# Performance work log

Measured on AMD Instinct MI355X. Metric: run time of the kernel, lower is better.

The kernel has to match this reference:

```python
import jax, jax.numpy as jnp
import numpy as np

H = 512      # hidden_size
GH = 512     # global_hidden_size
V = 128      # VOCAB_SIZE (one-hot arg_hot width)
D = 14       # tree depth; complete binary tree
NUM_OPS = 36
N_INT = 5    # num_internal_ops
N_NODES = 2 ** (D + 1) - 1  # 32767, heap layout: node i has children 2i+1, 2i+2


def _p(key, i, shape, s=0.05):
    return jax.random.normal(jax.random.fold_in(key, i), shape, dtype=jnp.float32) * s


def setup_inputs() -> dict:
    key = jax.random.key(0)
    return {
        "tokens": jax.random.randint(jax.random.fold_in(key, 0), (N_NODES,), 0, V),
        "validity_mask": jnp.ones((NUM_OPS,), jnp.float32),
        # binary tree-LSTM (blstm): 2 children
        "W_iou_b": _p(key, 1, (V, 3 * H)), "U_iou_b": _p(key, 2, (2, H, 3 * H)), "b_iou_b": jnp.zeros((3 * H,), jnp.float32),
        "Wf_b": _p(key, 3, (V, H)), "Uf_b": _p(key, 4, (2, H, H)), "bf_b": jnp.ones((H,), jnp.float32),
        # ternary tree-LSTM (tlstm): 3 children
        "W_iou_t": _p(key, 5, (V, 3 * H)), "U_iou_t": _p(key, 6, (3, H, 3 * H)), "b_iou_t": jnp.zeros((3 * H,), jnp.float32),
        "Wf_t": _p(key, 7, (V, H)), "Uf_t": _p(key, 8, (3, H, H)), "bf_t": jnp.ones((H,), jnp.float32),
        # FFN: one h-by-h layer (ffn_complexity = h^2 * n_layers, n_layers=1)
        "ffn_W": _p(key, 9, (H, H)), "ffn_b": jnp.zeros((H,), jnp.float32),
        # global LSTM (1 layer, 1 step), torch gate order i,f,g,o
        "lstm_Wx": _p(key, 10, (H, 4 * GH)), "lstm_Wh": _p(key, 11, (GH, 4 * GH)), "lstm_b": jnp.zeros((4 * GH,), jnp.float32),
        # actor heads on concat(root_hidden, h_glob)
        "hl_W": _p(key, 12, (H + GH, 2)), "hl_b": jnp.zeros((2,), jnp.float32),
        "int_W": _p(key, 13, (H + GH, N_INT)), "int_b": jnp.zeros((N_INT,), jnp.float32),
        "act_W": _p(key, 14, (H + GH, NUM_OPS)), "act_b": jnp.zeros((NUM_OPS,), jnp.float32),
    }


def _nary_cell(x, hk, ck, W_iou, U_iou, b_iou, Wf, Uf, bf):
    # x: [n, V]; hk, ck: [n, K, H]  (K children)
    iou = x @ W_iou + jnp.einsum('nkh,khg->ng', hk, U_iou) + b_iou
    i, o, u = jnp.split(iou, 3, axis=-1)
    f = jax.nn.sigmoid((x @ Wf + bf)[:, None, :] + jnp.einsum('nkh,khg->nkg', hk, Uf))
    c = jax.nn.sigmoid(i) * jnp.tanh(u) + jnp.sum(f * ck, axis=1)
    h = jax.nn.sigmoid(o) * jnp.tanh(c)
    return h, c


def _forward(tokens, validity_mask, W_iou_b, U_iou_b, b_iou_b, Wf_b, Uf_b, bf_b,
             W_iou_t, U_iou_t, b_iou_t, Wf_t, Uf_t, bf_t, ffn_W, ffn_b,
             lstm_Wx, lstm_Wh, lstm_b, hl_W, hl_b, int_W, int_b, act_W, act_b):
    arg_hot = jax.nn.one_hot(tokens, V, dtype=jnp.float32)  # [N_NODES, V]
    h_prev = c_prev = None
    h_ab = c_ab = None
    # apply_binary_lstm over the whole tree, bottom-up, one batched cell per level
    for lvl in range(D, -1, -1):
        n = 2 ** lvl
        x = arg_hot[n - 1:2 * n - 1]  # level lvl occupies heap slots [2^l-1, 2^{l+1}-2]
        if h_prev is None:
            hk = jnp.zeros((n, 2, H), jnp.float32)  # leaves: tz children
            ck = hk
        else:
            hk = h_prev.reshape(n, 2, H)
            ck = c_prev.reshape(n, 2, H)
        h_prev, c_prev = _nary_cell(x, hk, ck, W_iou_b, U_iou_b, b_iou_b, Wf_b, Uf_b, bf_b)
        if lvl == 1:
            h_ab, c_ab = h_prev, c_prev  # root's children a, b
    # apply_ternary_lstm at depth 0: children = (self.hidden, a.hidden, b.hidden)
    hk3 = jnp.concatenate([h_prev, h_ab], axis=0)[None]  # [1, 3, H]
    ck3 = jnp.concatenate([c_prev, c_ab], axis=0)[None]
    h_root, c_root = _nary_cell(arg_hot[0:1], hk3, ck3, W_iou_t, U_iou_t, b_iou_t, Wf_t, Uf_t, bf_t)
    # apply_ffn (1 layer) then apply_global_lstm (single step from zero state)
    h_f = jnp.maximum(h_root @ ffn_W + ffn_b, 0.0)  # [1, H]
    h_g = jnp.zeros((1, GH), jnp.float32)
    c_g = h_g
    gates = h_f @ lstm_Wx + h_g @ lstm_Wh + lstm_b
    gi, gf, gg, go = jnp.split(gates, 4, axis=-1)
    c_g = jax.nn.sigmoid(gf) * c_g + jax.nn.sigmoid(gi) * jnp.tanh(gg)
    h_g = jax.nn.sigmoid(go) * jnp.tanh(c_g)
    # actor heads
    feat = jnp.concatenate([h_f, h_g], axis=-1)  # [1, H+GH]
    hl = feat @ hl_W + hl_b
    il = feat @ int_W + int_b
    el = jnp.log(validity_mask)[None, :] + feat @ (act_W * validity_mask[None, :]) + act_b * validity_mask
    return jnp.concatenate([hl, il, el], axis=-1)  # [1, 2 + N_INT + NUM_OPS]


def reference(tokens, validity_mask, W_iou_b, U_iou_b, b_iou_b, Wf_b, Uf_b, bf_b,
              W_iou_t, U_iou_t, b_iou_t, Wf_t, Uf_t, bf_t, ffn_W, ffn_b,
              lstm_Wx, lstm_Wh, lstm_b, hl_W, hl_b, int_W, int_b, act_W, act_b):
    return _forward(tokens, validity_mask, W_iou_b, U_iou_b, b_iou_b, Wf_b, Uf_b, bf_b,
                    W_iou_t, U_iou_t, b_iou_t, Wf_t, Uf_t, bf_t, ffn_W, ffn_b,
                    lstm_Wx, lstm_Wh, lstm_b, hl_W, hl_b, int_W, int_b, act_W, act_b)
```

## Files before the change

kernel.cpp:

```cpp
#include <hip/hip_runtime.h>
#include <hip/hip_bf16.h>
#include <math.h>

#define H 512
#define V 128
#define NLEAF 16384

typedef __attribute__((ext_vector_type(4))) float f32x4;
typedef __attribute__((ext_vector_type(8))) short s16x8;
typedef __attribute__((ext_vector_type(4))) unsigned short u16x4;
typedef unsigned short ushort_t;

__device__ ushort_t g_hb0[NLEAF * H];
__device__ ushort_t g_hb1[(NLEAF / 2) * H];
__device__ float    g_c0[NLEAF * H];
__device__ float    g_c1[(NLEAF / 2) * H];
__device__ __align__(16) ushort_t g_htab[V * H];
__device__ __align__(16) float    g_ctab[V * H];
__device__ __align__(16) float    g_Wpack[V * H * 4];
__device__ __align__(16) float    g_Uh0[V * 3 * H];
__device__ __align__(16) float    g_Uh1[V * 3 * H];
__device__ __align__(16) float    g_Vf0[V * H];
__device__ __align__(16) float    g_Vf1[V * H];
__device__ __align__(16) float    g_uhp[4 * 2 * V * 2048];
__device__ ushort_t g_UiouT[3 * H * 2 * H];
__device__ ushort_t g_UfT[H * 2 * H];
__device__ __align__(16) ushort_t g_Ustage[8 * 16 * 32 * 64 * 8];
__device__ ushort_t g_UiouTt[3 * H * 3 * H];
__device__ ushort_t g_UfTt[H * 3 * H];
__device__ float    g_rpart[3 * 3072];
__device__ float    g_hf[H];
__device__ float    g_gates[4 * H];

__device__ __forceinline__ float sigm(float x) { return 1.0f / (1.0f + __expf(-x)); }
__device__ __forceinline__ float ftanh(float x) {
  return 1.0f - 2.0f / (__expf(2.0f * x) + 1.0f);
}
__device__ __forceinline__ ushort_t f2bf(float x) {
  __hip_bfloat16 b = __float2bfloat16(x);
  return *reinterpret_cast<ushort_t*>(&b);
}
__device__ __forceinline__ float bf2f(ushort_t u) {
  union { unsigned int i; float f; } v; v.i = ((unsigned int)u) << 16; return v.f;
}
__device__ __forceinline__ void gload_lds16(const void* g, void* l) {
  __builtin_amdgcn_global_load_lds(
      (const __attribute__((address_space(1))) unsigned int*)g,
      (__attribute__((address_space(3))) unsigned int*)l, 16, 0, 0);
}
#define WAITV(N) asm volatile("s_waitcnt vmcnt(" #N ")" ::: "memory")

__global__ __launch_bounds__(256) void k_prep(
    const float* __restrict__ s0, const float* __restrict__ s1,
    const float* __restrict__ s2, const float* __restrict__ s3,
    ushort_t* __restrict__ d0, ushort_t* __restrict__ d1,
    ushort_t* __restrict__ d2, ushort_t* __restrict__ d3,
    const float* __restrict__ Wiou, const float* __restrict__ biou,
    const float* __restrict__ Wf, const float* __restrict__ bf) {
  if (blockIdx.z == 4) {
    const int v = blockIdx.y * 48 + blockIdx.x;
    if (v >= V) return;
    for (int j = threadIdx.x; j < H; j += 256) {
      float wi = Wiou[(size_t)v * 1536 + j] + biou[j];
      float wo = Wiou[(size_t)v * 1536 + 512 + j] + biou[512 + j];
      float wu = Wiou[(size_t)v * 1536 + 1024 + j] + biou[1024 + j];
      float wf = Wf[(size_t)v * 512 + j] + bf[j];
      f32x4 wp = {wi, wo, wu, wf};
      *reinterpret_cast<f32x4*>(&g_Wpack[((size_t)v * 512 + j) * 4]) = wp;
      float c = sigm(wi) * ftanh(wu);
      float h = sigm(wo) * ftanh(c);
      g_htab[v * H + j] = f2bf(h);
      g_ctab[v * H + j] = c;
    }
    return;
  }
  const float* src; ushort_t* dst; int R, Cc;
  switch (blockIdx.z) {
    case 0: src = s0; dst = d0; R = 1024; Cc = 1536; break;
    case 1: src = s1; dst = d1; R = 1024; Cc = 512; break;
    case 2: src = s2; dst = d2; R = 1536; Cc = 1536; break;
    default: src = s3; dst = d3; R = 1536; Cc = 512; break;
  }
  int bc = blockIdx.x * 32, br = blockIdx.y * 32;
  if (bc >= Cc || br >= R) return;
  __shared__ float t[32][33];
  int tx = threadIdx.x & 31, ty = threadIdx.x >> 5;
  for (int rr = ty; rr < 32; rr += 8)
    t[rr][tx] = src[(size_t)(br + rr) * Cc + bc + tx];
  __syncthreads();
  for (int rr = ty; rr < 32; rr += 8)
    dst[(size_t)(bc + rr) * R + br + tx] = f2bf(t[tx][rr]);
}

__global__ __launch_bounds__(256) void k_packU(const float* __restrict__ Uiou,
                                               const float* __restrict__ Uf) {
  const int jb = blockIdx.x;
  const int ct = blockIdx.y;
  const int kz = blockIdx.z;
  const int t = threadIdx.x;
  const int kt = kz * 4 + (t >> 6);
  const int lane = t & 63;
  const int colu = ct * 16 + (lane & 15);
  const int g = colu >> 6;
  const int jj = jb * 64 + (colu & 63);
  const int kbase = kt * 32 + ((lane >> 4) << 3);
  u16x4 v0, v1;
  #pragma unroll
  for (int r = 0; r < 8; ++r) {
    int k = kbase + r;
    float v = (g < 3) ? Uiou[(size_t)k * 1536 + g * 512 + jj]
                      : Uf[(size_t)k * 512 + jj];
    if (r < 4) v0[r] = f2bf(v); else v1[r - 4] = f2bf(v);
  }
  ushort_t* dst = g_Ustage + (((size_t)(jb * 16 + ct) * 32 + kt) * 64 + lane) * 8;
  *reinterpret_cast<u16x4*>(dst) = v0;
  *reinterpret_cast<u16x4*>(dst + 4) = v1;
}

__global__ __launch_bounds__(256) void k_uhg() {
  const int cb0 = blockIdx.x * 64;
  const int kh = blockIdx.y;
  const int kc = blockIdx.z;
  const int tid = threadIdx.x;
  const int lane = tid & 63;
  const int w = tid >> 6;
  const int wry = w >> 1;
  const int cx = w & 1;

  __shared__ f32x4 suv[3072];
  char* smem = (char*)suv;

  const unsigned kA = (unsigned)(kc * 256) + ((lane >> 4) * 16);
  const unsigned kB = (unsigned)(kh * 1024) + kA;
  #pragma unroll
  for (int uu = 0; uu < 3; ++uu) {
    int u = w * 3 + uu;
    const char* base;
    unsigned dstb;
    if (u < 8) {
      int row = u * 16 + (lane & 15);
      base = (const char*)g_htab + (size_t)row * 1024 + kA;
      dstb = (unsigned)u * 4096u;
    } else {
      int col = cb0 + (u - 8) * 16 + (lane & 15);
      const ushort_t* cp = (col < 1536) ? (g_UiouT + (size_t)col * 1024)
                                        : (g_UfT + (size_t)(col - 1536) * 1024);
      base = (const char*)cp + kB;
      dstb = 32768u + (unsigned)(u - 8) * 4096u;
    }
    #pragma unroll
    for (int kt = 0; kt < 4; ++kt)
      gload_lds16(base + kt * 64, smem + dstb + kt * 1024u);
  }
  WAITV(0);
  __syncthreads();

  f32x4 acc[4][2];
  #pragma unroll
  for (int a = 0; a < 4; ++a) { acc[a][0] = (f32x4){0,0,0,0}; acc[a][1] = (f32x4){0,0,0,0}; }

  #pragma unroll
  for (int kt = 0; kt < 4; ++kt) {
    const char* ab = smem + wry * 16384 + kt * 1024 + lane * 16;
    const char* bb = smem + 32768 + cx * 8192 + kt * 1024 + lane * 16;
    s16x8 b0 = *(const s16x8*)(bb);
    s16x8 b1 = *(const s16x8*)(bb + 4096);
    #pragma unroll
    for (int rtl = 0; rtl < 4; ++rtl) {
      s16x8 av = *(const s16x8*)(ab + rtl * 4096);
      acc[rtl][0] = __builtin_amdgcn_mfma_f32_16x16x32_bf16(av, b0, acc[rtl][0], 0, 0, 0);
      acc[rtl][1] = __builtin_amdgcn_mfma_f32_16x16x32_bf16(av, b1, acc[rtl][1], 0, 0, 0);
    }
  }

  float* outb = g_uhp + ((size_t)(kc * 2 + kh) * V) * 2048;
  #pragma unroll
  for (int rtl = 0; rtl < 4; ++rtl) {
    #pragma unroll
    for (int t = 0; t < 2; ++t) {
      int col = cb0 + cx * 32 + t * 16 + (lane & 15);
      int vb = wry * 64 + rtl * 16 + (lane >> 4) * 4;
      #pragma unroll
      for (int r = 0; r < 4; ++r)
        outb[(size_t)(vb + r) * 2048 + col] = acc[rtl][t][r];
    }
  }
}

__global__ __launch_bounds__(256) void k_uhred() {
  int e = blockIdx.x * 256 + threadIdx.x;
  float s = g_uhp[e] + g_uhp[524288 + e] + g_uhp[2 * 524288 + e]
          + g_uhp[3 * 524288 + e];
  int kh = e >> 18;
  int rem = e & 262143;
  int v = rem >> 11;
  int c = rem & 2047;
  if (c < 1536) (kh ? g_Uh1 : g_Uh0)[(size_t)v * 1536 + c] = s;
  else          (kh ? g_Vf1 : g_Vf0)[(size_t)v * 512 + (c - 1536)] = s;
}

__global__ __launch_bounds__(256) void k_top_cell(const int* __restrict__ tokens) {
  const int total = 8192 * 128;
  for (int q = blockIdx.x * 256 + threadIdx.x; q < total; q += gridDim.x * 256) {
    int i = q >> 7, jv = q & 127;
    int t0 = tokens[(NLEAF - 1) + 2 * i];
    int t1 = tokens[(NLEAF - 1) + 2 * i + 1];
    int tk = tokens[8191 + i];
    const f32x4* u0 = (const f32x4*)&g_Uh0[(size_t)t0 * 1536];
    const f32x4* u1 = (const f32x4*)&g_Uh1[(size_t)t1 * 1536];
    f32x4 ii = u0[jv] + u1[jv];
    f32x4 oo = u0[128 + jv] + u1[128 + jv];
    f32x4 uu = u0[256 + jv] + u1[256 + jv];
    f32x4 v0 = ((const f32x4*)&g_Vf0[(size_t)t0 * 512])[jv];
    f32x4 v1 = ((const f32x4*)&g_Vf1[(size_t)t1 * 512])[jv];
    f32x4 c0 = ((const f32x4*)&g_ctab[(size_t)t0 * 512])[jv];
    f32x4 c1 = ((const f32x4*)&g_ctab[(size_t)t1 * 512])[jv];
    const f32x4* wpp = (const f32x4*)g_Wpack + (size_t)tk * 512 + jv * 4;
    u16x4 hv; f32x4 cv;
    #pragma unroll
    for (int r = 0; r < 4; ++r) {
      f32x4 wp = wpp[r];
      float ig = ii[r] + wp[0];
      float og = oo[r] + wp[1];
      float ug = uu[r] + wp[2];
      float fp = wp[3];
      float cc = sigm(ig) * ftanh(ug) + sigm(fp + v0[r]) * c0[r]
               + sigm(fp + v1[r]) * c1[r];
      float hh = sigm(og) * ftanh(cc);
      cv[r] = cc;
      hv[r] = f2bf(hh);
    }
    *reinterpret_cast<u16x4*>(&g_hb1[(size_t)q * 4]) = hv;
    *reinterpret_cast<f32x4*>(&g_c1[(size_t)q * 4]) = cv;
  }
}

#define COMPUTE64(FA, S)                                                     \
  {                                                                          \
    const char* ab = smem + buf * 16384 + wry * 8192 + (S) * 1024 + lane * 16; \
    s16x8 a0 = *(const s16x8*)(ab);                                          \
    s16x8 a1 = *(const s16x8*)(ab + 2048);                                   \
    s16x8 a2 = *(const s16x8*)(ab + 4096);                                   \
    s16x8 a3 = *(const s16x8*)(ab + 6144);                                   \
    const char* bb = smem + 32768 + buf * 32768 + cx * 4096 + (S) * 1024 + lane * 16; \
    s16x8 b0 = *(const s16x8*)(bb);                                          \
    s16x8 b1 = *(const s16x8*)(bb + 2048);                                   \
    s16x8 b2 = *(const s16x8*)(bb + 8192);                                   \
    s16x8 b3 = *(const s16x8*)(bb + 10240);                                  \
    s16x8 b4 = *(const s16x8*)(bb + 16384);                                  \
    s16x8 b5 = *(const s16x8*)(bb + 18432);                                  \
    s16x8 b6 = *(const s16x8*)(bb + 24576);                                  \
    s16x8 b7 = *(const s16x8*)(bb + 26624);                                  \
    s16x8 aa[4] = {a0, a1, a2, a3};                                          \
    _Pragma("unroll")                                                        \
    for (int rtl = 0; rtl < 4; ++rtl) {                                      \
      acc[rtl][0] = __builtin_amdgcn_mfma_f32_16x16x32_bf16(aa[rtl], b0, acc[rtl][0], 0, 0, 0); \
      acc[rtl][1] = __builtin_amdgcn_mfma_f32_16x16x32_bf16(aa[rtl], b1, acc[rtl][1], 0, 0, 0); \
      acc[rtl][2] = __builtin_amdgcn_mfma_f32_16x16x32_bf16(aa[rtl], b2, acc[rtl][2], 0, 0, 0); \
      acc[rtl][3] = __builtin_amdgcn_mfma_f32_16x16x32_bf16(aa[rtl], b3, acc[rtl][3], 0, 0, 0); \
      acc[rtl][4] = __builtin_amdgcn_mfma_f32_16x16x32_bf16(aa[rtl], b4, acc[rtl][4], 0, 0, 0); \
      acc[rtl][5] = __builtin_amdgcn_mfma_f32_16x16x32_bf16(aa[rtl], b5, acc[rtl][5], 0, 0, 0); \
      acc[rtl][FA] = __builtin_amdgcn_mfma_f32_16x16x32_bf16(aa[rtl], b6, acc[rtl][FA], 0, 0, 0); \
      acc[rtl][FA + 1] = __builtin_amdgcn_mfma_f32_16x16x32_bf16(aa[rtl], b7, acc[rtl][FA + 1], 0, 0, 0); \
    }                                                                        \
  }

__global__ __launch_bounds__(256, 1) void k_mfma_rest(int lvl,
    const int* __restrict__ tokens) {
  const int n = 1 << lvl;
  const int node0 = n - 1;
  const int outp = lvl & 1;
  const ushort_t* __restrict__ hprev = outp ? g_hb0 : g_hb1;
  const float* __restrict__ cprev = outp ? g_c0 : g_c1;
  ushort_t* __restrict__ hout = outp ? g_hb1 : g_hb0;
  float* __restrict__ cout = outp ? g_c1 : g_c0;

  const int i0 = blockIdx.x * 128;
  const int j0 = blockIdx.y * 64;
  const int tid = threadIdx.x;
  const int lane = tid & 63;
  const int w = tid >> 6;
  const int wry = w >> 1;
  const int cx = w & 1;

  __shared__ f32x4 smemv[6144];
  char* smem = (char*)smemv;

  const char* gp[6];
  unsigned lb[6], lstr[6], off2[6], adv[6];
  {
    int kb = (lane >> 4) * 16;
    #pragma unroll
    for (int q = 0; q < 6; ++q) {
      int c = w * 6 + q;
      if (c < 8) {
        int row = i0 + c * 16 + (lane & 15);
        gp[q] = (const char*)hprev + (size_t)row * 2048 + kb;
        lb[q] = c * 2048u; lstr[q] = 16384u; off2[q] = 64u; adv[q] = 128u;
      } else {
        int ct = c - 8;
        gp[q] = (const char*)g_Ustage +
                ((size_t)(blockIdx.y * 16 + ct) << 15) + lane * 16;
        lb[q] = 32768u + ct * 2048u; lstr[q] = 32768u;
        off2[q] = 1024u; adv[q] = 2048u;
      }
    }
  }

#define STAGE2(BUF)                                                          \
  {                                                                          \
    _Pragma("unroll")                                                        \
    for (int q = 0; q < 6; ++q) {                                            \
      gload_lds16(gp[q], smem + lb[q] + (unsigned)(BUF) * lstr[q]);          \
      gload_lds16(gp[q] + off2[q],                                           \
                  smem + lb[q] + (unsigned)(BUF) * lstr[q] + 1024u);         \
      gp[q] += adv[q];                                                       \
    }                                                                        \
  }

  f32x4 acc[4][10];
  #pragma unroll
  for (int a = 0; a < 4; ++a)
    #pragma unroll
    for (int b = 0; b < 10; ++b) acc[a][b] = (f32x4){0.f, 0.f, 0.f, 0.f};

  STAGE2(0); STAGE2(1);
  int buf = 0;
  for (int ph = 0; ph < 8; ++ph) {
    WAITV(12);
    __builtin_amdgcn_s_barrier();
    COMPUTE64(6, 0);
    COMPUTE64(6, 1);
    __builtin_amdgcn_s_barrier();
    STAGE2(buf);
    buf ^= 1;
  }
  for (int ph = 8; ph < 14; ++ph) {
    WAITV(12);
    __builtin_amdgcn_s_barrier();
    COMPUTE64(8, 0);
    COMPUTE64(8, 1);
    __builtin_amdgcn_s_barrier();
    STAGE2(buf);
    buf ^= 1;
  }
  WAITV(12); __builtin_amdgcn_s_barrier();
  COMPUTE64(8, 0); COMPUTE64(8, 1);
  buf ^= 1;
  WAITV(0); __builtin_amdgcn_s_barrier();
  COMPUTE64(8, 0); COMPUTE64(8, 1);
#undef STAGE2

  const int node_c = lane >> 4;
  const int jl = lane & 15;
  #pragma unroll
  for (int t = 0; t < 2; ++t) {
    const int j = j0 + cx * 32 + t * 16 + jl;
    #pragma unroll
    for (int rtl = 0; rtl < 4; ++rtl) {
      f32x4 vi = acc[rtl][0 + t], vo = acc[rtl][2 + t], vu = acc[rtl][4 + t],
            v0 = acc[rtl][6 + t], v1 = acc[rtl][8 + t];
      const int ib = i0 + wry * 64 + rtl * 16 + node_c * 4;
      #pragma unroll
      for (int r = 0; r < 4; ++r) {
        int i = ib + r;
        int tok = tokens[node0 + i];
        f32x4 wp = ((const f32x4*)g_Wpack)[(size_t)tok * 512 + j];
        float ig = vi[r] + wp[0];
        float og = vo[r] + wp[1];
        float ug = vu[r] + wp[2];
        float fpre = wp[3];
        float cc = sigm(ig) * ftanh(ug)
                 + sigm(fpre + v0[r]) * cprev[(size_t)(2 * i) * 512 + j]
                 + sigm(fpre + v1[r]) * cprev[(size_t)(2 * i + 1) * 512 + j];
        float hh = sigm(og) * ftanh(cc);
        hout[(size_t)i * 512 + j] = f2bf(hh);
        cout[(size_t)i * 512 + j] = cc;
      }
    }
  }
}

__global__ __launch_bounds__(256) void k_small(int lvl,
    const int* __restrict__ tokens) {
  const int n = 1 << lvl;
  const int node0 = n - 1;
  const int outp = lvl & 1;
  const ushort_t* __restrict__ hprev = outp ? g_hb0 : g_hb1;
  const float* __restrict__ cprev = outp ? g_c0 : g_c1;
  ushort_t* __restrict__ hout = outp ? g_hb1 : g_hb0;
  float* __restrict__ cout = outp ? g_c1 : g_c0;

  const int i = blockIdx.y;
  const int j0 = blockIdx.x * 64;
  const int tid = threadIdx.x;
  const int lane = tid & 63;
  const int w = tid >> 6;

  __shared__ float exch[5][64];

  float hv[16];
  {
    const s16x8* hp = (const s16x8*)(hprev + (size_t)i * 1024 + lane * 16);
    s16x8 h0 = hp[0], h1 = hp[1];
    #pragma unroll
    for (int r = 0; r < 8; ++r) {
      hv[r] = bf2f((ushort_t)h0[r]);
      hv[8 + r] = bf2f((ushort_t)h1[r]);
    }
  }

  for (int u = w; u < 256; u += 4) {
    int jc = u & 63, g = u >> 6, jj = j0 + jc;
    const ushort_t* col = (g < 3) ? (g_UiouT + (size_t)(g * 512 + jj) * 1024)
                                  : (g_UfT + (size_t)jj * 1024);
    const s16x8* cp = (const s16x8*)(col + lane * 16);
    s16x8 w0 = cp[0], w1 = cp[1];
    float s = 0.f;
    #pragma unroll
    for (int r = 0; r < 8; ++r) {
      s += bf2f((ushort_t)w0[r]) * hv[r];
      s += bf2f((ushort_t)w1[r]) * hv[8 + r];
    }
    s += __shfl_xor(s, 1);
    s += __shfl_xor(s, 2);
    s += __shfl_xor(s, 4);
    s += __shfl_xor(s, 8);
    s += __shfl_xor(s, 16);
    if (g < 3) {
      s += __shfl_xor(s, 32);
      if (lane == 0) exch[g][jc] = s;
    } else {
      if (lane == 0) exch[3][jc] = s;
      if (lane == 32) exch[4][jc] = s;
    }
  }
  __syncthreads();

  if (tid < 64) {
    int j = j0 + tid;
    int tok = tokens[node0 + i];
    f32x4 wp = ((const f32x4*)g_Wpack)[(size_t)tok * 512 + j];
    float ig = exch[0][tid] + wp[0];
    float og = exch[1][tid] + wp[1];
    float ug = exch[2][tid] + wp[2];
    float fpre = wp[3];
    float cc = sigm(ig) * ftanh(ug)
             + sigm(fpre + exch[3][tid]) * cprev[(size_t)(2 * i) * 512 + j]
             + sigm(fpre + exch[4][tid]) * cprev[(size_t)(2 * i + 1) * 512 + j];
    float hh = sigm(og) * ftanh(cc);
    hout[(size_t)i * 512 + j] = f2bf(hh);
    cout[(size_t)i * 512 + j] = cc;
  }
}

__global__ __launch_bounds__(256) void k_root_p1() {
  const int by = blockIdx.y;
  const int tid = threadIdx.x;
  const int lane = tid & 63;
  const int w = tid >> 6;
  const int cbase = blockIdx.x * 256;

  float hv[8];
  {
    int m0 = by * 512 + lane * 8;
    #pragma unroll
    for (int r = 0; r < 8; ++r) {
      int m = m0 + r;
      hv[r] = (m < 512) ? bf2f(g_hb0[m]) : bf2f(g_hb1[m - 512]);
    }
  }

  for (int u = w; u < 256; u += 4) {
    int c = cbase + u;
    const ushort_t* col = nullptr;
    if (c < 1536) {
      col = g_UiouTt + (size_t)c * 1536 + by * 512;
    } else {
      int v = c - 1536;
      if ((v >> 9) == by) col = g_UfTt + (size_t)(v & 511) * 1536 + by * 512;
    }
    float s = 0.f;
    if (col) {
      s16x8 wv = *(const s16x8*)(col + lane * 8);
      #pragma unroll
      for (int r = 0; r < 8; ++r) s += bf2f((ushort_t)wv[r]) * hv[r];
    }
    s += __shfl_xor(s, 1);
    s += __shfl_xor(s, 2);
    s += __shfl_xor(s, 4);
    s += __shfl_xor(s, 8);
    s += __shfl_xor(s, 16);
    s += __shfl_xor(s, 32);
    if (lane == 0) g_rpart[(size_t)by * 3072 + c] = s;
  }
}

__global__ __launch_bounds__(512) void k_p2h1(const int* __restrict__ tokens,
    const float* __restrict__ Wiou_t, const float* __restrict__ biou_t,
    const float* __restrict__ Wf_t, const float* __restrict__ bf_t,
    const float* __restrict__ ffnW, const float* __restrict__ ffnb) {
  __shared__ float hroot[H];
  const int j = threadIdx.x;
  float ai = g_rpart[j] + g_rpart[3072 + j] + g_rpart[6144 + j];
  float ao = g_rpart[512 + j] + g_rpart[3072 + 512 + j] + g_rpart[6144 + 512 + j];
  float au = g_rpart[1024 + j] + g_rpart[3072 + 1024 + j] + g_rpart[6144 + 1024 + j];
  float f0 = g_rpart[1536 + j] + g_rpart[3072 + 1536 + j] + g_rpart[6144 + 1536 + j];
  float f1 = g_rpart[2048 + j] + g_rpart[3072 + 2048 + j] + g_rpart[6144 + 2048 + j];
  float f2 = g_rpart[2560 + j] + g_rpart[3072 + 2560 + j] + g_rpart[6144 + 2560 + j];

  int tok = tokens[0];
  float fpre = Wf_t[(size_t)tok * H + j] + bf_t[j];
  float ig = ai + Wiou_t[(size_t)tok * 3 * H + j] + biou_t[j];
  float og = ao + Wiou_t[(size_t)tok * 3 * H + H + j] + biou_t[H + j];
  float ug = au + Wiou_t[(size_t)tok * 3 * H + 2 * H + j] + biou_t[2 * H + j];
  float cc = sigm(ig) * ftanh(ug)
           + sigm(fpre + f0) * g_c0[j]
           + sigm(fpre + f1) * g_c1[j]
           + sigm(fpre + f2) * g_c1[H + j];
  hroot[j] = sigm(og) * ftanh(cc);
  __syncthreads();

  float acc = ffnb[j];
  #pragma unroll 8
  for (int m = 0; m < H; ++m) acc += hroot[m] * ffnW[m * H + j];
  g_hf[j] = fmaxf(acc, 0.0f);
}

__global__ __launch_bounds__(64) void k_head2(const float* __restrict__ Wx,
                                              const float* __restrict__ lb) {
  int idx = blockIdx.x * 64 + threadIdx.x;
  int region = idx >> 9;
  int j = idx & 511;
  int g2 = (region == 0) ? j : ((region == 1) ? 1024 + j : 1536 + j);
  float acc = lb[g2];
  #pragma unroll 8
  for (int m = 0; m < H; ++m) acc += g_hf[m] * Wx[m * 4 * H + g2];
  g_gates[g2] = acc;
}

__global__ __launch_bounds__(512) void k_head3(const float* __restrict__ vm,
    const float* __restrict__ hlW, const float* __restrict__ hlb,
    const float* __restrict__ intW, const float* __restrict__ intb,
    const float* __restrict__ actW, const float* __restrict__ actb,
    float* __restrict__ out) {
  __shared__ float feat[2 * H];
  int j = threadIdx.x;
  float ci = sigm(g_gates[j]) * ftanh(g_gates[2 * H + j]);
  float hg = sigm(g_gates[3 * H + j]) * ftanh(ci);
  feat[j] = g_hf[j];
  feat[H + j] = hg;
  __syncthreads();

  const int wv = threadIdx.x >> 6;
  const int lane = threadIdx.x & 63;
  for (int o = wv; o < 43; o += 8) {
    const float* Wc;
    int stride, colb;
    if (o < 2)       { Wc = hlW;  stride = 2;  colb = o; }
    else if (o < 7)  { Wc = intW; stride = 5;  colb = o - 2; }
    else             { Wc = actW; stride = 36; colb = o - 7; }
    float s = 0.f;
    #pragma unroll
    for (int q = 0; q < 16; ++q) {
      int m = lane + q * 64;
      s += feat[m] * Wc[(size_t)m * stride + colb];
    }
    #pragma unroll
    for (int d = 32; d >= 1; d >>= 1) s += __shfl_xor(s, d);
    if (lane == 0) {
      float res;
      if (o < 2)      res = s + hlb[o];
      else if (o < 7) res = s + intb[o - 2];
      else {
        int a = o - 7;
        float v = vm[a];
        res = __logf(v) + s * v + actb[a] * v;
      }
      out[o] = res;
    }
  }
}

extern "C" void kernel_launch(void* const* d_in, const int* in_sizes, int n_in,
                              void* d_out, int out_size, void* d_ws, size_t ws_size,
                              hipStream_t stream) {
  (void)in_sizes; (void)n_in; (void)d_ws; (void)ws_size; (void)out_size;
  const int* tokens   = (const int*)d_in[0];
  const float* vm     = (const float*)d_in[1];
  const float* Wiou_b = (const float*)d_in[2];
  const float* Uiou_b = (const float*)d_in[3];
  const float* biou_b = (const float*)d_in[4];
  const float* Wf_b   = (const float*)d_in[5];
  const float* Uf_b   = (const float*)d_in[6];
  const float* bf_b   = (const float*)d_in[7];
  const float* Wiou_t = (const float*)d_in[8];
  const float* Uiou_t = (const float*)d_in[9];
  const float* biou_t = (const float*)d_in[10];
  const float* Wf_t   = (const float*)d_in[11];
  const float* Uf_t   = (const float*)d_in[12];
  const float* bf_t   = (const float*)d_in[13];
  const float* ffnW   = (const float*)d_in[14];
  const float* ffnb   = (const float*)d_in[15];
  const float* lstmWx = (const float*)d_in[16];
  const float* lstmb  = (const float*)d_in[18];
  const float* hlW    = (const float*)d_in[19];
  const float* hlb    = (const float*)d_in[20];
  const float* intW   = (const float*)d_in[21];
  const float* intb   = (const float*)d_in[22];
  const float* actW   = (const float*)d_in[23];
  const float* actb   = (const float*)d_in[24];

  ushort_t* UiouT;  hipGetSymbolAddress((void**)&UiouT, HIP_SYMBOL(g_UiouT));
  ushort_t* UfT;    hipGetSymbolAddress((void**)&UfT, HIP_SYMBOL(g_UfT));
  ushort_t* UiouTt; hipGetSymbolAddress((void**)&UiouTt, HIP_SYMBOL(g_UiouTt));
  ushort_t* UfTt;   hipGetSymbolAddress((void**)&UfTt, HIP_SYMBOL(g_UfTt));

  k_prep<<<dim3(48, 48, 5), 256, 0, stream>>>(
      Uiou_b, Uf_b, Uiou_t, Uf_t, UiouT, UfT, UiouTt, UfTt,
      Wiou_b, biou_b, Wf_b, bf_b);
  k_packU<<<dim3(8, 16, 8), 256, 0, stream>>>(Uiou_b, Uf_b);

  k_uhg<<<dim3(32, 2, 4), 256, 0, stream>>>();
  k_uhred<<<2048, 256, 0, stream>>>();
  k_top_cell<<<2048, 256, 0, stream>>>(tokens);

  for (int lvl = 12; lvl >= 8; --lvl) {
    int gx = (1 << lvl) / 128;
    k_mfma_rest<<<dim3(gx, 8), 256, 0, stream>>>(lvl, tokens);
  }
  for (int lvl = 7; lvl >= 0; --lvl) {
    int n = 1 << lvl;
    k_small<<<dim3(8, n), 256, 0, stream>>>(lvl, tokens);
  }
  k_root_p1<<<dim3(12, 3), 256, 0, stream>>>();
  k_p2h1<<<1, 512, 0, stream>>>(tokens, Wiou_t, biou_t, Wf_t, bf_t, ffnW, ffnb);
  k_head2<<<24, 64, 0, stream>>>(lstmWx, lstmb);
  k_head3<<<1, 512, 0, stream>>>(vm, hlW, hlb, intW, intb, actW, actb, (float*)d_out);
}
```

Measured before the change: 685.3 us.

## Split K across wave pairs in MFMA level kernel with LDS reduction

The per-level MFMA kernel moves from 256 to 512 threads. Each pair of waves splits the K dimension and reduces partial accumulators through shared memory before the gate epilogue. The double-buffered pipelined staging is replaced by single-buffer 4-slice loads with full barriers each phase. The aim is more waves per CU on small grids, at the cost of less load/compute overlap and an extra LDS reduction. k_packU now reads from the already transposed bf16 U copies instead of strided fp32 loads.

```diff
diff --git a/kernel.cpp b/kernel.cpp
--- a/kernel.cpp
+++ b/kernel.cpp
@@ -92,27 +92,20 @@
     dst[(size_t)(bc + rr) * R + br + tx] = f2bf(t[tx][rr]);
 }
 
-__global__ __launch_bounds__(256) void k_packU(const float* __restrict__ Uiou,
-                                               const float* __restrict__ Uf) {
-  const int jb = blockIdx.x;
-  const int ct = blockIdx.y;
-  const int kz = blockIdx.z;
-  const int t = threadIdx.x;
-  const int kt = kz * 4 + (t >> 6);
-  const int lane = t & 63;
+__global__ __launch_bounds__(256) void k_packU() {
+  const int tile = blockIdx.x;
+  const int jb = tile >> 4, ct = tile & 15;
+  const int kt = blockIdx.y * 4 + (threadIdx.x >> 6);
+  const int lane = threadIdx.x & 63;
   const int colu = ct * 16 + (lane & 15);
   const int g = colu >> 6;
   const int jj = jb * 64 + (colu & 63);
-  const int kbase = kt * 32 + ((lane >> 4) << 3);
-  u16x4 v0, v1;
-  #pragma unroll
-  for (int r = 0; r < 8; ++r) {
-    int k = kbase + r;
-    float v = (g < 3) ? Uiou[(size_t)k * 1536 + g * 512 + jj]
-                      : Uf[(size_t)k * 512 + jj];
-    if (r < 4) v0[r] = f2bf(v); else v1[r - 4] = f2bf(v);
-  }
-  ushort_t* dst = g_Ustage + (((size_t)(jb * 16 + ct) * 32 + kt) * 64 + lane) * 8;
+  const int k = kt * 32 + ((lane >> 4) << 3);
+  const ushort_t* src = (g < 3) ? (g_UiouT + (size_t)(g * 512 + jj) * 1024 + k)
+                                : (g_UfT + (size_t)jj * 1024 + k);
+  u16x4 v0 = *reinterpret_cast<const u16x4*>(src);
+  u16x4 v1 = *reinterpret_cast<const u16x4*>(src + 4);
+  ushort_t* dst = g_Ustage + (((size_t)tile * 32 + kt) * 64 + lane) * 8;
   *reinterpret_cast<u16x4*>(dst) = v0;
   *reinterpret_cast<u16x4*>(dst + 4) = v1;
 }
@@ -235,22 +228,22 @@
   }
 }
 
-#define COMPUTE64(FA, S)                                                     \
+#define CPH(FA, S)                                                           \
   {                                                                          \
-    const char* ab = smem + buf * 16384 + wry * 8192 + (S) * 1024 + lane * 16; \
+    const char* ab = smem + wry * 16384 + (S) * 1024 + lane * 16;            \
     s16x8 a0 = *(const s16x8*)(ab);                                          \
-    s16x8 a1 = *(const s16x8*)(ab + 2048);                                   \
-    s16x8 a2 = *(const s16x8*)(ab + 4096);                                   \
-    s16x8 a3 = *(const s16x8*)(ab + 6144);                                   \
-    const char* bb = smem + 32768 + buf * 32768 + cx * 4096 + (S) * 1024 + lane * 16; \
+    s16x8 a1 = *(const s16x8*)(ab + 4096);                                   \
+    s16x8 a2 = *(const s16x8*)(ab + 8192);                                   \
+    s16x8 a3 = *(const s16x8*)(ab + 12288);                                  \
+    const char* bb = smem + 32768 + cx * 8192 + (S) * 1024 + lane * 16;      \
     s16x8 b0 = *(const s16x8*)(bb);                                          \
-    s16x8 b1 = *(const s16x8*)(bb + 2048);                                   \
-    s16x8 b2 = *(const s16x8*)(bb + 8192);                                   \
-    s16x8 b3 = *(const s16x8*)(bb + 10240);                                  \
-    s16x8 b4 = *(const s16x8*)(bb + 16384);                                  \
-    s16x8 b5 = *(const s16x8*)(bb + 18432);                                  \
-    s16x8 b6 = *(const s16x8*)(bb + 24576);                                  \
-    s16x8 b7 = *(const s16x8*)(bb + 26624);                                  \
+    s16x8 b1 = *(const s16x8*)(bb + 4096);                                   \
+    s16x8 b2 = *(const s16x8*)(bb + 16384);                                  \
+    s16x8 b3 = *(const s16x8*)(bb + 20480);                                  \
+    s16x8 b4 = *(const s16x8*)(bb + 32768);                                  \
+    s16x8 b5 = *(const s16x8*)(bb + 36864);                                  \
+    s16x8 b6 = *(const s16x8*)(bb + 49152);                                  \
+    s16x8 b7 = *(const s16x8*)(bb + 53248);                                  \
     s16x8 aa[4] = {a0, a1, a2, a3};                                          \
     _Pragma("unroll")                                                        \
     for (int rtl = 0; rtl < 4; ++rtl) {                                      \
@@ -265,7 +258,7 @@
     }                                                                        \
   }
 
-__global__ __launch_bounds__(256, 1) void k_mfma_rest(int lvl,
+__global__ __launch_bounds__(512, 1) void k_mfma_rest(int lvl,
     const int* __restrict__ tokens) {
   const int n = 1 << lvl;
   const int node0 = n - 1;
@@ -280,42 +273,32 @@
   const int tid = threadIdx.x;
   const int lane = tid & 63;
   const int w = tid >> 6;
-  const int wry = w >> 1;
-  const int cx = w & 1;
+  const int kz = w & 1;
+  const int cx = (w >> 1) & 1;
+  const int wry = w >> 2;
 
   __shared__ f32x4 smemv[6144];
   char* smem = (char*)smemv;
 
-  const char* gp[6];
-  unsigned lb[6], lstr[6], off2[6], adv[6];
+  const char* gp[12];
+  unsigned adv[12], dsto[12];
   {
-    int kb = (lane >> 4) * 16;
-    #pragma unroll
-    for (int q = 0; q < 6; ++q) {
-      int c = w * 6 + q;
-      if (c < 8) {
-        int row = i0 + c * 16 + (lane & 15);
-        gp[q] = (const char*)hprev + (size_t)row * 2048 + kb;
-        lb[q] = c * 2048u; lstr[q] = 16384u; off2[q] = 64u; adv[q] = 128u;
+    #pragma unroll
+    for (int q = 0; q < 12; ++q) {
+      int c = w * 12 + q;
+      dsto[q] = (unsigned)c * 1024u + (unsigned)lane * 16u;
+      if (c < 32) {
+        int rt = c >> 2, S = c & 3;
+        gp[q] = (const char*)hprev + (size_t)(i0 + rt * 16 + (lane & 15)) * 2048
+              + S * 64 + ((lane >> 4) * 16);
+        adv[q] = 256u;
       } else {
-        int ct = c - 8;
-        gp[q] = (const char*)g_Ustage +
-                ((size_t)(blockIdx.y * 16 + ct) << 15) + lane * 16;
-        lb[q] = 32768u + ct * 2048u; lstr[q] = 32768u;
-        off2[q] = 1024u; adv[q] = 2048u;
+        int u = (c - 32) >> 2, S = (c - 32) & 3;
+        gp[q] = (const char*)g_Ustage + ((size_t)(blockIdx.y * 16 + u) << 15)
+              + (unsigned)S * 1024u + (unsigned)lane * 16u;
+        adv[q] = 4096u;
       }
     }
-  }
-
-#define STAGE2(BUF)                                                          \
-  {                                                                          \
-    _Pragma("unroll")                                                        \
-    for (int q = 0; q < 6; ++q) {                                            \
-      gload_lds16(gp[q], smem + lb[q] + (unsigned)(BUF) * lstr[q]);          \
-      gload_lds16(gp[q] + off2[q],                                           \
-                  smem + lb[q] + (unsigned)(BUF) * lstr[q] + 1024u);         \
-      gp[q] += adv[q];                                                       \
-    }                                                                        \
   }
 
   f32x4 acc[4][10];
@@ -324,58 +307,82 @@
     #pragma unroll
     for (int b = 0; b < 10; ++b) acc[a][b] = (f32x4){0.f, 0.f, 0.f, 0.f};
 
-  STAGE2(0); STAGE2(1);
-  int buf = 0;
-  for (int ph = 0; ph < 8; ++ph) {
-    WAITV(12);
-    __builtin_amdgcn_s_barrier();
-    COMPUTE64(6, 0);
-    COMPUTE64(6, 1);
-    __builtin_amdgcn_s_barrier();
-    STAGE2(buf);
-    buf ^= 1;
-  }
-  for (int ph = 8; ph < 14; ++ph) {
-    WAITV(12);
-    __builtin_amdgcn_s_barrier();
-    COMPUTE64(8, 0);
-    COMPUTE64(8, 1);
-    __builtin_amdgcn_s_barrier();
-    STAGE2(buf);
-    buf ^= 1;
-  }
-  WAITV(12); __builtin_amdgcn_s_barrier();
-  COMPUTE64(8, 0); COMPUTE64(8, 1);
-  buf ^= 1;
-  WAITV(0); __builtin_amdgcn_s_barrier();
-  COMPUTE64(8, 0); COMPUTE64(8, 1);
-#undef STAGE2
-
-  const int node_c = lane >> 4;
-  const int jl = lane & 15;
-  #pragma unroll
-  for (int t = 0; t < 2; ++t) {
-    const int j = j0 + cx * 32 + t * 16 + jl;
-    #pragma unroll
-    for (int rtl = 0; rtl < 4; ++rtl) {
-      f32x4 vi = acc[rtl][0 + t], vo = acc[rtl][2 + t], vu = acc[rtl][4 + t],
-            v0 = acc[rtl][6 + t], v1 = acc[rtl][8 + t];
-      const int ib = i0 + wry * 64 + rtl * 16 + node_c * 4;
+  const int S0 = kz * 2;
+  for (int p = 0; p < 4; ++p) {
+    __syncthreads();
+    #pragma unroll
+    for (int q = 0; q < 12; ++q) { gload_lds16(gp[q], smem + dsto[q]); gp[q] += adv[q]; }
+    WAITV(0);
+    __syncthreads();
+    CPH(6, S0);
+    CPH(6, S0 + 1);
+  }
+  for (int p = 4; p < 8; ++p) {
+    __syncthreads();
+    #pragma unroll
+    for (int q = 0; q < 12; ++q) { gload_lds16(gp[q], smem + dsto[q]); gp[q] += adv[q]; }
+    WAITV(0);
+    __syncthreads();
+    CPH(8, S0);
+    CPH(8, S0 + 1);
+  }
+
+  f32x4* cb = (f32x4*)smem;
+  const int slot = (wry * 2 + cx) * 64 + lane;
+  __syncthreads();
+  if (kz) {
+    #pragma unroll
+    for (int rtl = 0; rtl < 2; ++rtl)
       #pragma unroll
-      for (int r = 0; r < 4; ++r) {
-        int i = ib + r;
-        int tok = tokens[node0 + i];
-        f32x4 wp = ((const f32x4*)g_Wpack)[(size_t)tok * 512 + j];
-        float ig = vi[r] + wp[0];
-        float og = vo[r] + wp[1];
-        float ug = vu[r] + wp[2];
-        float fpre = wp[3];
-        float cc = sigm(ig) * ftanh(ug)
-                 + sigm(fpre + v0[r]) * cprev[(size_t)(2 * i) * 512 + j]
-                 + sigm(fpre + v1[r]) * cprev[(size_t)(2 * i + 1) * 512 + j];
-        float hh = sigm(og) * ftanh(cc);
-        hout[(size_t)i * 512 + j] = f2bf(hh);
-        cout[(size_t)i * 512 + j] = cc;
+      for (int b = 0; b < 10; ++b) cb[(rtl * 10 + b) * 256 + slot] = acc[rtl][b];
+  }
+  __syncthreads();
+  if (!kz) {
+    #pragma unroll
+    for (int rtl = 0; rtl < 2; ++rtl)
+      #pragma unroll
+      for (int b = 0; b < 10; ++b) acc[rtl][b] += cb[(rtl * 10 + b) * 256 + slot];
+  }
+  __syncthreads();
+  if (kz) {
+    #pragma unroll
+    for (int rtl = 2; rtl < 4; ++rtl)
+      #pragma unroll
+      for (int b = 0; b < 10; ++b) cb[((rtl - 2) * 10 + b) * 256 + slot] = acc[rtl][b];
+  }
+  __syncthreads();
+  if (!kz) {
+    #pragma unroll
+    for (int rtl = 2; rtl < 4; ++rtl)
+      #pragma unroll
+      for (int b = 0; b < 10; ++b) acc[rtl][b] += cb[((rtl - 2) * 10 + b) * 256 + slot];
+
+    const int node_c = lane >> 4;
+    const int jl = lane & 15;
+    #pragma unroll
+    for (int t = 0; t < 2; ++t) {
+      const int j = j0 + cx * 32 + t * 16 + jl;
+      #pragma unroll
+      for (int rtl = 0; rtl < 4; ++rtl) {
+        f32x4 vi = acc[rtl][0 + t], vo = acc[rtl][2 + t], vu = acc[rtl][4 + t],
+              v0 = acc[rtl][6 + t], v1 = acc[rtl][8 + t];
+        const int ib = i0 + wry * 64 + rtl * 16 + node_c * 4;
+        #pragma unroll
+        for (int r = 0; r < 4; ++r) {
+          int i = ib + r;
+          int tok = tokens[node0 + i];
+          f32x4 wp = ((const f32x4*)g_Wpack)[(size_t)tok * 512 + j];
+          float ig = vi[r] + wp[0];
+          float og = vo[r] + wp[1];
+          float ug = vu[r] + wp[2];
+          float fpre = wp[3];
+          float cc = sigm(ig) * ftanh(ug)
+                   + sigm(fpre + v0[r]) * cprev[(size_t)(2 * i) * 512 + j]
+                   + sigm(fpre + v1[r]) * cprev[(size_t)(2 * i + 1) * 512 + j];
+          float hh = sigm(og) * ftanh(cc);
+          hout[(size_t)i * 512 + j] = f2bf(hh);
+          cout[(size_t)i * 512 + j] = cc;
+        }
       }
     }
   }
@@ -619,7 +626,7 @@
   k_prep<<<dim3(48, 48, 5), 256, 0, stream>>>(
       Uiou_b, Uf_b, Uiou_t, Uf_t, UiouT, UfT, UiouTt, UfTt,
       Wiou_b, biou_b, Wf_b, bf_b);
-  k_packU<<<dim3(8, 16, 8), 256, 0, stream>>>(Uiou_b, Uf_b);
+  k_packU<<<dim3(128, 8), 256, 0, stream>>>();
 
   k_uhg<<<dim3(32, 2, 4), 256, 0, stream>>>();
   k_uhred<<<2048, 256, 0, stream>>>();
@@ -627,7 +634,7 @@
 
   for (int lvl = 12; lvl >= 8; --lvl) {
     int gx = (1 << lvl) / 128;
-    k_mfma_rest<<<dim3(gx, 8), 256, 0, stream>>>(lvl, tokens);
+    k_mfma_rest<<<dim3(gx, 8), 512, 0, stream>>>(lvl, tokens);
   }
   for (int lvl = 7; lvl >= 0; --lvl) {
     int n = 1 << lvl;
```

Measured after the change: 642.7 us. -6.2%, faster.
